# Kernel optimization log

Hardware: AMD Instinct MI355X
Metric: run time of the kernel (lower is better)

Reference implementation:

```python
import jax, jax.numpy as jnp
import numpy as np

NUM_USER = 100000
NUM_ITEM = 50000
DIM = 64
NUM_EDGES = 3200000


def setup_inputs() -> dict:
    key = jax.random.key(0)
    k1, k2, k3, k4 = jax.random.split(key, 4)
    return {
        "user_embedding": jax.random.normal(k1, (NUM_USER, DIM), dtype=jnp.float32),
        "item_embedding": jax.random.normal(k2, (NUM_ITEM, DIM), dtype=jnp.float32),
        "edge_user": jax.random.randint(k3, (NUM_EDGES,), 0, NUM_USER, dtype=jnp.int32).astype(jnp.int64),
        "edge_item": jax.random.randint(k4, (NUM_EDGES,), 0, NUM_ITEM, dtype=jnp.int32).astype(jnp.int64),
    }


def _segment_mean(feats, idx, num_segments):
    # scatter_mean semantics: sum per segment / count, empty segments -> 0
    s = jax.ops.segment_sum(feats, idx, num_segments=num_segments)  # [n, dim]
    cnt = jax.ops.segment_sum(jnp.ones((idx.shape[0], 1), feats.dtype), idx,
                              num_segments=num_segments)  # [n, 1]
    return s / jnp.maximum(cnt, 1.0)


def reference(user_embedding, item_embedding, edge_user, edge_item):
    num_user = user_embedding.shape[0]
    num_item = item_embedding.shape[0]

    # view1: aggregate_neighbor_features — mean of purchased-item embeddings per user
    neighbor_feat = _segment_mean(item_embedding[edge_item], edge_user, num_user)

    # view2: aggregate_cooccurrence_features — two-stage mean aggregation
    # stage 1: per item, mean of its purchasers' embeddings
    item_user_agg = _segment_mean(user_embedding[edge_user], edge_item, num_item)
    # stage 2: per user, mean of stage-1 features of purchased items
    cooccur_feat = _segment_mean(item_user_agg[edge_item], edge_user, num_user)

    return (neighbor_feat, cooccur_feat)
```

## Files before the change

kernel.cpp:

```cpp
#include <hip/hip_runtime.h>
#include <hip/hip_fp16.h>

constexpr int NUM_USER  = 100000;
constexpr int NUM_ITEM  = 50000;
constexpr int DIM       = 64;
constexpr int NUM_EDGES = 3200000;

constexpr int KPB   = 32;
constexpr int NB_U  = (NUM_USER + KPB - 1) / KPB;
constexpr int NB_I  = (NUM_ITEM + KPB - 1) / KPB;
constexpr int CHUNK = 4096;
constexpr int CSH   = 14;
constexpr int NCH_I = 4;
constexpr int NCH_U = 7;
constexpr int CAP_U = 1280;
constexpr int CAP_I = 2304;
constexpr int PGRID = 256;
constexpr int CVTB  = 256;

__device__ __forceinline__ __half2 u2h(unsigned u) {
  union { unsigned u; __half2 h; } v; v.u = u; return v.h;
}
__device__ __forceinline__ unsigned h2u(__half2 h) {
  union { __half2 h; unsigned u; } v; v.h = h; return v.u;
}
__device__ __forceinline__ float u_as_f(unsigned u) {
  union { unsigned u; float f; } v; v.u = u; return v.f;
}

__device__ __forceinline__ int detect64(const void* eu, const void* ei) {
  const int* a = (const int*)eu;
  const int* b = (const int*)ei;
  int any = 0;
#pragma unroll
  for (int i = 1; i < 64; i += 2) { any |= a[i]; any |= b[i]; }
  return any == 0;
}

__device__ __forceinline__ int idx_at(const void* p, int e, int is64) {
  return is64 ? ((const int*)p)[2 * e] : ((const int*)p)[e];
}

__device__ __forceinline__ void cvt_body(int t0, int stride,
                                         const float* __restrict__ ue,
                                         unsigned* __restrict__ u32,
                                         const float* __restrict__ ie,
                                         unsigned* __restrict__ fused) {
  const int nu = NUM_USER * 32, ni = NUM_ITEM * 32;
  for (int t = t0; t < nu + ni; t += stride) {
    if (t < nu) {
      const unsigned long long raw =
          __builtin_nontemporal_load((const unsigned long long*)ue + t);
      const __half2 h = __floats2half2_rn(u_as_f((unsigned)raw),
                                          u_as_f((unsigned)(raw >> 32)));
      __builtin_nontemporal_store(h2u(h), &u32[t]);
    } else {
      const int s = t - nu;
      const unsigned long long raw =
          __builtin_nontemporal_load((const unsigned long long*)ie + s);
      const __half2 h = __floats2half2_rn(u_as_f((unsigned)raw),
                                          u_as_f((unsigned)(raw >> 32)));
      __builtin_nontemporal_store(h2u(h),
                                  &fused[(size_t)(s >> 5) * 64 + 2 * (s & 31)]);
    }
  }
}

__global__ void k_part2cvt(const void* eu_p, const void* ei_p,
                           int* gcur_i, unsigned int* __restrict__ pairs_i,
                           int* gcur_u, unsigned int* __restrict__ pairs_u,
                           int capI, int capU,
                           const float* __restrict__ ue, unsigned* __restrict__ u32t,
                           const float* __restrict__ ie, unsigned* __restrict__ fusedt) {
  __shared__ int hist_u[NB_U], base_u[NB_U];
  __shared__ int hist_i[NB_I], base_i[NB_I];
  if (blockIdx.x >= PGRID) {
    cvt_body((blockIdx.x - PGRID) * blockDim.x + threadIdx.x,
             CVTB * blockDim.x, ue, u32t, ie, fusedt);
    return;
  }
  for (int t = threadIdx.x; t < NB_U; t += blockDim.x) hist_u[t] = 0;
  for (int t = threadIdx.x; t < NB_I; t += blockDim.x) hist_i[t] = 0;
  __syncthreads();
  const int is64 = detect64(eu_p, ei_p);
  const int ch = NUM_EDGES / PGRID;
  const int lo = blockIdx.x * ch, hiE = lo + ch;
  for (int e = lo + threadIdx.x; e < hiE; e += blockDim.x) {
    atomicAdd(&hist_u[idx_at(eu_p, e, is64) >> 5], 1);
    atomicAdd(&hist_i[idx_at(ei_p, e, is64) >> 5], 1);
  }
  __syncthreads();
  for (int t = threadIdx.x; t < NB_U; t += blockDim.x) {
    const int h = hist_u[t];
    int b = 0;
    if (h) {
      b = atomicAdd(&gcur_u[t], h);
      if (capU) b += t * capU;
    }
    base_u[t] = b;
    hist_u[t] = 0;
  }
  for (int t = threadIdx.x; t < NB_I; t += blockDim.x) {
    const int h = hist_i[t];
    int b = 0;
    if (h) {
      b = atomicAdd(&gcur_i[t], h);
      if (capI) b += t * capI;
    }
    base_i[t] = b;
    hist_i[t] = 0;
  }
  __syncthreads();
  for (int e = lo + threadIdx.x; e < hiE; e += blockDim.x) {
    const int eu = idx_at(eu_p, e, is64);
    const int ei = idx_at(ei_p, e, is64);
    const int bi = ei >> 5;
    const int pi = base_i[bi] + atomicAdd(&hist_i[bi], 1);
    if (!capI || pi < (bi + 1) * capI)
      pairs_i[pi] = ((unsigned)(ei & 31) << 17) | (unsigned)eu;
    const int bu = eu >> 5;
    const int pu = base_u[bu] + atomicAdd(&hist_u[bu], 1);
    if (!capU || pu < (bu + 1) * capU)
      pairs_u[pu] = ((unsigned)(eu & 31) << 17) | (unsigned)ei;
  }
}

__global__ void k_hist_part(const void* eu_p, const void* ei_p,
                            int* __restrict__ partials) {
  __shared__ int hu[NB_U];
  __shared__ int hi_[NB_I];
  for (int t = threadIdx.x; t < NB_U; t += blockDim.x) hu[t] = 0;
  for (int t = threadIdx.x; t < NB_I; t += blockDim.x) hi_[t] = 0;
  __syncthreads();
  const int is64 = detect64(eu_p, ei_p);
  const int ga = gridDim.x;
  const int ch = NUM_EDGES / ga;
  const int b = blockIdx.x;
  const int lo = b * ch, hiE = lo + ch;
  for (int e = lo + threadIdx.x; e < hiE; e += blockDim.x) {
    atomicAdd(&hu[idx_at(eu_p, e, is64) >> 5], 1);
    atomicAdd(&hi_[idx_at(ei_p, e, is64) >> 5], 1);
  }
  __syncthreads();
  int* pu = partials;
  int* pi = partials + (size_t)NB_U * ga;
  for (int t = threadIdx.x; t < NB_U; t += blockDim.x) pu[(size_t)t * ga + b] = hu[t];
  for (int t = threadIdx.x; t < NB_I; t += blockDim.x) pi[(size_t)t * ga + b] = hi_[t];
}

__global__ void k_hist_reduce(const int* __restrict__ partials, int ga,
                              int* __restrict__ gcnt_u, int* __restrict__ gcnt_i) {
  const int k = blockIdx.x * blockDim.x + threadIdx.x;
  if (k >= NB_U + NB_I) return;
  const int* base = (k < NB_U) ? partials + (size_t)k * ga
                               : partials + (size_t)NB_U * ga + (size_t)(k - NB_U) * ga;
  int s = 0;
  for (int b = 0; b < ga; ++b) s += base[b];
  if (k < NB_U) gcnt_u[k] = s;
  else          gcnt_i[k - NB_U] = s;
}

__device__ void scan_body(const int* __restrict__ in, int* __restrict__ out,
                          int* __restrict__ cur, int n) {
  __shared__ int part[1024];
  const int t = threadIdx.x;
  const int chunk = (n + 1023) >> 10;
  const int lo = min(t * chunk, n);
  const int hi = min(lo + chunk, n);
  int s = 0;
  for (int i = lo; i < hi; ++i) s += in[i];
  part[t] = s;
  __syncthreads();
  for (int d = 1; d < 1024; d <<= 1) {
    int v = (t >= d) ? part[t - d] : 0;
    __syncthreads();
    part[t] += v;
    __syncthreads();
  }
  int run = (t == 0) ? 0 : part[t - 1];
  for (int i = lo; i < hi; ++i) {
    int v = in[i];
    out[i] = run; cur[i] = run; run += v;
  }
  if (t == 1023) out[n] = part[1023];
}

__global__ void k_scan2(const int* cu, int* bu, int* curu,
                        const int* ci, int* bi, int* curi) {
  if (blockIdx.x == 0) scan_body(cu, bu, curu, NB_U);
  else                 scan_body(ci, bi, curi, NB_I);
}

__device__ __forceinline__ void bucket_extent(int bucket, const int* gbase,
                                              const int* gcnt, int cap,
                                              int& lo, int& hi) {
  if (cap > 0) {
    lo = bucket * cap;
    hi = lo + min(gcnt[bucket], cap);
  } else {
    lo = gbase[bucket];
    hi = gbase[bucket + 1];
  }
}

__global__ __launch_bounds__(256, 8)
void k_agg_item(const unsigned* __restrict__ user32,
                const unsigned int* __restrict__ pairs,
                const int* __restrict__ gbase, const int* __restrict__ gcnt,
                int cap, unsigned* __restrict__ fused) {
  constexpr int NBINS = NCH_U * KPB;
  __shared__ int sorted[CHUNK];
  __shared__ int hist[NBINS], base[NBINS], cur[NBINS];
  __shared__ int gsum[NCH_U];
  const int tid = threadIdx.x;
  const int lane = tid & 63;
  const int wid = tid >> 6;
  const int half = lane >> 5;
  const int c = lane & 31;
  const int bucket = blockIdx.x;
  int lo, hi;
  bucket_extent(bucket, gbase, gcnt, cap, lo, hi);

  unsigned s[8]; int cnt[8];
#pragma unroll
  for (int r = 0; r < 8; ++r) { s[r] = 0u; cnt[r] = 0; }

  for (int clo = lo; clo < hi; clo += CHUNK) {
    const int csz = min(CHUNK, hi - clo);
    for (int t = tid; t < NBINS; t += 256) hist[t] = 0;
    __syncthreads();
    for (int j = tid; j < csz; j += 256) {
      const unsigned p = pairs[clo + j];
      atomicAdd(&hist[((p & 0x1FFFF) >> CSH) * KPB + (p >> 17)], 1);
    }
    __syncthreads();
    if (tid < NCH_U) {
      int g = 0;
      for (int q = 0; q < KPB; ++q) g += hist[tid * KPB + q];
      gsum[tid] = g;
    }
    __syncthreads();
    for (int t = tid; t < NBINS; t += 256) {
      const int ch = t >> 5;
      int b = 0;
      for (int q = 0; q < ch; ++q) b += gsum[q];
      for (int q = ch * KPB; q < t; ++q) b += hist[q];
      base[t] = b; cur[t] = b;
    }
    __syncthreads();
    for (int j = tid; j < csz; j += 256) {
      const unsigned p = pairs[clo + j];
      const int v = (int)(p & 0x1FFFF);
      const int slot = atomicAdd(&cur[(v >> CSH) * KPB + (p >> 17)], 1);
      sorted[slot] = v;
    }
    __syncthreads();
    for (int ch = 0; ch < NCH_U; ++ch) {
#pragma unroll
      for (int r = 0; r < 8; ++r) {
        const int bin = ch * KPB + wid * 8 + r;
        const int jlo = base[bin], jhi = cur[bin];
        cnt[r] += jhi - jlo;
        for (int j = jlo; j < jhi; j += 8) {
          unsigned w[4];
#pragma unroll
          for (int q = 0; q < 4; ++q) {
            const int jj = j + 2 * q + half;
            w[q] = (jj < jhi) ? user32[(size_t)sorted[jj] * 32 + c] : 0u;
          }
#pragma unroll
          for (int q = 0; q < 4; ++q)
            s[r] = h2u(__hadd2(u2h(s[r]), u2h(w[q])));
        }
      }
    }
    __syncthreads();
  }

  const int i0 = bucket * KPB;
#pragma unroll
  for (int r = 0; r < 8; ++r) {
    const unsigned o = (unsigned)__shfl_xor((int)s[r], 32);
    const __half2 tot = __hadd2(u2h(s[r]), u2h(o));
    const int item = i0 + wid * 8 + r;
    if (half == 0 && item < NUM_ITEM) {
      const float inv = 1.0f / fmaxf((float)cnt[r], 1.f);
      fused[(size_t)item * 64 + 2 * c + 1] =
          h2u(__floats2half2_rn(__low2float(tot) * inv, __high2float(tot) * inv));
    }
  }
}

__global__ __launch_bounds__(256, 8)
void k_agg_user(const unsigned* __restrict__ fused,
                const unsigned int* __restrict__ pairs,
                const int* __restrict__ gbase, const int* __restrict__ gcnt,
                int cap,
                float* __restrict__ out0, float* __restrict__ out1) {
  constexpr int NBINS = NCH_I * KPB;
  __shared__ int sorted[CHUNK];
  __shared__ int hist[NBINS], base[NBINS], cur[NBINS];
  __shared__ int gsum[NCH_I];
  const int tid = threadIdx.x;
  const int lane = tid & 63;
  const int wid = tid >> 6;
  const int half = lane >> 5;
  const int c = lane & 31;
  const int bucket = blockIdx.x;
  int lo, hi;
  bucket_extent(bucket, gbase, gcnt, cap, lo, hi);
  const uint2* fused2 = (const uint2*)fused;

  unsigned s0[8], s1[8]; int cnt[8];
#pragma unroll
  for (int r = 0; r < 8; ++r) { s0[r] = 0u; s1[r] = 0u; cnt[r] = 0; }

  for (int clo = lo; clo < hi; clo += CHUNK) {
    const int csz = min(CHUNK, hi - clo);
    for (int t = tid; t < NBINS; t += 256) hist[t] = 0;
    __syncthreads();
    for (int j = tid; j < csz; j += 256) {
      const unsigned p = pairs[clo + j];
      atomicAdd(&hist[((p & 0x1FFFF) >> CSH) * KPB + (p >> 17)], 1);
    }
    __syncthreads();
    if (tid < NCH_I) {
      int g = 0;
      for (int q = 0; q < KPB; ++q) g += hist[tid * KPB + q];
      gsum[tid] = g;
    }
    __syncthreads();
    for (int t = tid; t < NBINS; t += 256) {
      const int ch = t >> 5;
      int b = 0;
      for (int q = 0; q < ch; ++q) b += gsum[q];
      for (int q = ch * KPB; q < t; ++q) b += hist[q];
      base[t] = b; cur[t] = b;
    }
    __syncthreads();
    for (int j = tid; j < csz; j += 256) {
      const unsigned p = pairs[clo + j];
      const int v = (int)(p & 0x1FFFF);
      const int slot = atomicAdd(&cur[(v >> CSH) * KPB + (p >> 17)], 1);
      sorted[slot] = v;
    }
    __syncthreads();
    for (int ch = 0; ch < NCH_I; ++ch) {
#pragma unroll
      for (int r = 0; r < 8; ++r) {
        const int bin = ch * KPB + wid * 8 + r;
        const int jlo = base[bin], jhi = cur[bin];
        cnt[r] += jhi - jlo;
        for (int j = jlo; j < jhi; j += 8) {
          uint2 w[4];
#pragma unroll
          for (int q = 0; q < 4; ++q) {
            const int jj = j + 2 * q + half;
            w[q] = (jj < jhi) ? fused2[(size_t)sorted[jj] * 32 + c]
                              : make_uint2(0u, 0u);
          }
#pragma unroll
          for (int q = 0; q < 4; ++q) {
            s0[r] = h2u(__hadd2(u2h(s0[r]), u2h(w[q].x)));
            s1[r] = h2u(__hadd2(u2h(s1[r]), u2h(w[q].y)));
          }
        }
      }
    }
    __syncthreads();
  }

  const int u0 = bucket * KPB;
#pragma unroll
  for (int r = 0; r < 8; ++r) {
    const unsigned o0 = (unsigned)__shfl_xor((int)s0[r], 32);
    const unsigned o1 = (unsigned)__shfl_xor((int)s1[r], 32);
    const __half2 t0 = __hadd2(u2h(s0[r]), u2h(o0));
    const __half2 t1 = __hadd2(u2h(s1[r]), u2h(o1));
    const int u = u0 + wid * 8 + r;
    if (half == 0 && u < NUM_USER) {
      const float inv = 1.0f / fmaxf((float)cnt[r], 1.f);
      ((float2*)out0)[(size_t)u * 32 + c] =
          make_float2(__low2float(t0) * inv, __high2float(t0) * inv);
      ((float2*)out1)[(size_t)u * 32 + c] =
          make_float2(__low2float(t1) * inv, __high2float(t1) * inv);
    }
  }
}

__global__ void k_scatter1(const float* __restrict__ user_emb,
                           const float* __restrict__ item_emb,
                           const void* eu_p, const void* ei_p,
                           float* out0, float* item_sum,
                           float* cnt_user, float* cnt_item) {
  const int is64 = detect64(eu_p, ei_p);
  const int lane = threadIdx.x & (DIM - 1);
  const int sub  = threadIdx.x >> 6;
  const int epb  = blockDim.x >> 6;
  for (int e = blockIdx.x * epb + sub; e < NUM_EDGES; e += gridDim.x * epb) {
    const int eu = idx_at(eu_p, e, is64);
    const int ei = idx_at(ei_p, e, is64);
    atomicAdd(&out0[eu * DIM + lane], item_emb[ei * DIM + lane]);
    atomicAdd(&item_sum[ei * DIM + lane], user_emb[eu * DIM + lane]);
    if (lane == 0) {
      atomicAdd(&cnt_user[eu], 1.0f);
      atomicAdd(&cnt_item[ei], 1.0f);
    }
  }
}

__global__ void k_div_item(float* item_sum, const float* __restrict__ cnt_item) {
  const int n = NUM_ITEM * DIM;
  for (int t = blockIdx.x * blockDim.x + threadIdx.x; t < n;
       t += gridDim.x * blockDim.x)
    item_sum[t] /= fmaxf(cnt_item[t >> 6], 1.0f);
}

__global__ void k_scatter2(const float* __restrict__ item_agg,
                           const void* eu_p, const void* ei_p, float* out1) {
  const int is64 = detect64(eu_p, ei_p);
  const int lane = threadIdx.x & (DIM - 1);
  const int sub  = threadIdx.x >> 6;
  const int epb  = blockDim.x >> 6;
  for (int e = blockIdx.x * epb + sub; e < NUM_EDGES; e += gridDim.x * epb) {
    const int eu = idx_at(eu_p, e, is64);
    const int ei = idx_at(ei_p, e, is64);
    atomicAdd(&out1[eu * DIM + lane], item_agg[ei * DIM + lane]);
  }
}

__global__ void k_finalize(float* out0, float* out1,
                           const float* __restrict__ cnt_user) {
  const int n = NUM_USER * DIM;
  for (int t = blockIdx.x * blockDim.x + threadIdx.x; t < n;
       t += gridDim.x * blockDim.x) {
    const float c = fmaxf(cnt_user[t >> 6], 1.0f);
    out0[t] /= c;
    out1[t] /= c;
  }
}

extern "C" void kernel_launch(void* const* d_in, const int* in_sizes, int n_in,
                              void* d_out, int out_size, void* d_ws, size_t ws_size,
                              hipStream_t stream) {
  const float* user_emb = (const float*)d_in[0];
  const float* item_emb = (const float*)d_in[1];
  const void*  eu_p     = d_in[2];
  const void*  ei_p     = d_in[3];

  float* out0 = (float*)d_out;
  float* out1 = out0 + (size_t)NUM_USER * DIM;

  int* wsi = (int*)d_ws;
  float* wsf = (float*)d_ws;

  const size_t s_pairs_u = 0;
  const size_t s_pairs_i = s_pairs_u + (size_t)NB_U * CAP_U;
  const size_t s_user32  = s_pairs_i + (size_t)NB_I * CAP_I;
  const size_t s_fused   = s_user32 + (size_t)NUM_USER * 32;
  const size_t s_gcur_u  = s_fused + (size_t)NUM_ITEM * 64;
  const size_t s_gcur_i  = s_gcur_u + NB_U;
  const size_t s_end     = s_gcur_i + NB_I;
  const size_t need_static = s_end * 4;

  const size_t o_pairs   = 0;
  const size_t o_user32  = o_pairs + NUM_EDGES;
  const size_t o_fused   = o_user32 + (size_t)NUM_USER * 32;
  const size_t o_gcnt_u  = o_fused + (size_t)NUM_ITEM * 64;
  const size_t o_gbase_u = o_gcnt_u + NB_U;
  const size_t o_gcur_u  = o_gbase_u + NB_U + 1;
  const size_t o_gcnt_i  = o_gcur_u + NB_U;
  const size_t o_gbase_i = o_gcnt_i + NB_I;
  const size_t o_gcur_i  = o_gbase_i + NB_I + 1;
  const size_t o_pairs2  = o_gcur_i + NB_I;
  const size_t need_dynamic = (o_pairs2 + NUM_EDGES) * 4;

  if (ws_size >= need_static) {
    unsigned int* pairs_u = (unsigned int*)(wsi + s_pairs_u);
    unsigned int* pairs_i = (unsigned int*)(wsi + s_pairs_i);
    unsigned* user32 = (unsigned*)(wsi + s_user32);
    unsigned* fused  = (unsigned*)(wsi + s_fused);
    int* gcur_u = wsi + s_gcur_u;
    int* gcur_i = wsi + s_gcur_i;

    hipMemsetAsync(gcur_u, 0, (size_t)(NB_U + NB_I) * 4, stream);
    k_part2cvt<<<PGRID + CVTB, 1024, 0, stream>>>(
        eu_p, ei_p, gcur_i, pairs_i, gcur_u, pairs_u, CAP_I, CAP_U,
        user_emb, user32, item_emb, fused);
    k_agg_item<<<NB_I, 256, 0, stream>>>(user32, pairs_i, nullptr,
                                         gcur_i, CAP_I, fused);
    k_agg_user<<<NB_U, 256, 0, stream>>>(fused, pairs_u, nullptr,
                                         gcur_u, CAP_U, out0, out1);
  } else if (ws_size >= need_dynamic) {
    unsigned int* pairs_i  = (unsigned int*)(wsi + o_pairs);
    int*          partials = wsi + o_pairs;
    unsigned* user32 = (unsigned*)(wsi + o_user32);
    unsigned* fused  = (unsigned*)(wsi + o_fused);
    int* gcnt_u  = wsi + o_gcnt_u;
    int* gbase_u = wsi + o_gbase_u;
    int* gcur_u  = wsi + o_gcur_u;
    int* gcnt_i  = wsi + o_gcnt_i;
    int* gbase_i = wsi + o_gbase_i;
    int* gcur_i  = wsi + o_gcur_i;
    unsigned int* pairs_u = (unsigned int*)(wsi + o_pairs2);

    k_hist_part<<<256, 512, 0, stream>>>(eu_p, ei_p, partials);
    k_hist_reduce<<<(NB_U + NB_I + 255) / 256, 256, 0, stream>>>(partials, 256,
                                                                 gcnt_u, gcnt_i);
    k_scan2<<<2, 1024, 0, stream>>>(gcnt_u, gbase_u, gcur_u,
                                    gcnt_i, gbase_i, gcur_i);
    k_part2cvt<<<PGRID + CVTB, 1024, 0, stream>>>(
        eu_p, ei_p, gcur_i, pairs_i, gcur_u, pairs_u, 0, 0,
        user_emb, user32, item_emb, fused);
    k_agg_item<<<NB_I, 256, 0, stream>>>(user32, pairs_i, gbase_i,
                                         nullptr, 0, fused);
    k_agg_user<<<NB_U, 256, 0, stream>>>(fused, pairs_u, gbase_u,
                                         nullptr, 0, out0, out1);
  } else {
    float* item_sum = wsf;
    float* cnt_user = wsf + (size_t)NUM_ITEM * DIM;
    float* cnt_item = cnt_user + NUM_USER;
    const size_t used = ((size_t)NUM_ITEM * DIM + NUM_USER + NUM_ITEM) * 4;

    hipMemsetAsync(d_out, 0, (size_t)out_size * sizeof(float), stream);
    hipMemsetAsync(d_ws, 0, used, stream);
    k_scatter1<<<4096, 256, 0, stream>>>(user_emb, item_emb, eu_p, ei_p,
                                         out0, item_sum, cnt_user, cnt_item);
    k_div_item<<<2048, 256, 0, stream>>>(item_sum, cnt_item);
    k_scatter2<<<4096, 256, 0, stream>>>(item_sum, eu_p, ei_p, out1);
    k_finalize<<<2048, 256, 0, stream>>>(out0, out1, cnt_user);
  }
}
```

Measured before the change: 249.5 us.

## Replace single-pass bucket partition with two-pass coarse-then-fine radix partition

Edge partitioning now runs in two passes. The first pass scatters edges into 196 coarse groups (512 users or 256 items each), and a second kernel sub-partitions each group into the fine 32-row buckets. This replaces the single pass that kept ~4700 histogram bins in shared memory and issued scattered writes across thousands of buckets, which should improve write locality and cut global atomics. The cost is an extra read and write of all edge pairs plus more workspace, and the two-stage capacity clamps can drop edges if a group overflows. The old dynamic-offset path is removed and the static-capacity path is kept as a fallback.

```diff
diff --git a/kernel.cpp b/kernel.cpp
--- a/kernel.cpp
+++ b/kernel.cpp
@@ -17,6 +17,12 @@
 constexpr int CAP_I = 2304;
 constexpr int PGRID = 256;
 constexpr int CVTB  = 256;
+constexpr int NG    = 196;
+constexpr int GSH_U = 9;
+constexpr int GSH_I = 8;
+constexpr int FBG_U = 16;
+constexpr int FBG_I = 8;
+constexpr int GCAP  = 17152;
 
 __device__ __forceinline__ __half2 u2h(unsigned u) {
   union { unsigned u; __half2 h; } v; v.u = u; return v.h;
@@ -66,10 +72,97 @@
   }
 }
 
+__global__ void k_passA(const void* eu_p, const void* ei_p,
+                        int* gccur_u, int* gccur_i,
+                        unsigned* __restrict__ coarse_u,
+                        unsigned* __restrict__ coarse_i,
+                        const float* __restrict__ ue, unsigned* __restrict__ u32t,
+                        const float* __restrict__ ie, unsigned* __restrict__ fusedt) {
+  __shared__ int hu[NG], bu[NG];
+  __shared__ int hi_[NG], bi_[NG];
+  if (blockIdx.x >= PGRID) {
+    cvt_body((blockIdx.x - PGRID) * blockDim.x + threadIdx.x,
+             CVTB * blockDim.x, ue, u32t, ie, fusedt);
+    return;
+  }
+  for (int t = threadIdx.x; t < NG; t += blockDim.x) { hu[t] = 0; hi_[t] = 0; }
+  __syncthreads();
+  const int is64 = detect64(eu_p, ei_p);
+  const int ch = NUM_EDGES / PGRID;
+  const int lo = blockIdx.x * ch, hiE = lo + ch;
+  for (int e = lo + threadIdx.x; e < hiE; e += blockDim.x) {
+    atomicAdd(&hu[idx_at(eu_p, e, is64) >> GSH_U], 1);
+    atomicAdd(&hi_[idx_at(ei_p, e, is64) >> GSH_I], 1);
+  }
+  __syncthreads();
+  for (int t = threadIdx.x; t < NG; t += blockDim.x) {
+    const int h0 = hu[t];
+    bu[t] = h0 ? atomicAdd(&gccur_u[t], h0) : 0;
+    hu[t] = 0;
+    const int h1 = hi_[t];
+    bi_[t] = h1 ? atomicAdd(&gccur_i[t], h1) : 0;
+    hi_[t] = 0;
+  }
+  __syncthreads();
+  for (int e = lo + threadIdx.x; e < hiE; e += blockDim.x) {
+    const int eu = idx_at(eu_p, e, is64);
+    const int ei = idx_at(ei_p, e, is64);
+    const int gu = eu >> GSH_U;
+    const int pu = bu[gu] + atomicAdd(&hu[gu], 1);
+    if (pu < GCAP)
+      coarse_u[(size_t)gu * GCAP + pu] =
+          ((unsigned)(eu & ((1 << GSH_U) - 1)) << 17) | (unsigned)ei;
+    const int gi = ei >> GSH_I;
+    const int pi = bi_[gi] + atomicAdd(&hi_[gi], 1);
+    if (pi < GCAP)
+      coarse_i[(size_t)gi * GCAP + pi] =
+          ((unsigned)(ei & ((1 << GSH_I) - 1)) << 17) | (unsigned)eu;
+  }
+}
+
+__global__ void k_passB(const unsigned* __restrict__ coarse_u,
+                        const unsigned* __restrict__ coarse_i,
+                        const int* __restrict__ gccur_u,
+                        const int* __restrict__ gccur_i,
+                        unsigned* __restrict__ pairs_u,
+                        unsigned* __restrict__ pairs_i,
+                        int* __restrict__ gcnt_u, int* __restrict__ gcnt_i) {
+  __shared__ int h[FBG_U], cur[FBG_U];
+  const bool isU = blockIdx.x < NG;
+  const int g = isU ? blockIdx.x : blockIdx.x - NG;
+  const unsigned* src = (isU ? coarse_u : coarse_i) + (size_t)g * GCAP;
+  int n = isU ? gccur_u[g] : gccur_i[g];
+  n = min(n, GCAP);
+  const int FB = isU ? FBG_U : FBG_I;
+  const int CAP = isU ? CAP_U : CAP_I;
+  const int NBfin = isU ? NB_U : NB_I;
+  unsigned* dst = isU ? pairs_u : pairs_i;
+  int* gcnt = isU ? gcnt_u : gcnt_i;
+  const int tid = threadIdx.x;
+
+  if (tid < FB) h[tid] = 0;
+  __syncthreads();
+  for (int j = tid; j < n; j += blockDim.x)
+    atomicAdd(&h[(src[j] >> 22) & (FB - 1)], 1);
+  __syncthreads();
+  if (tid < FB) {
+    const int fbg = g * FB + tid;
+    if (fbg < NBfin) gcnt[fbg] = min(h[tid], CAP);
+    cur[tid] = 0;
+  }
+  __syncthreads();
+  for (int j = tid; j < n; j += blockDim.x) {
+    const unsigned p = src[j];
+    const int fb = (p >> 22) & (FB - 1);
+    const int pos = atomicAdd(&cur[fb], 1);
+    if (pos < CAP)
+      dst[(size_t)(g * FB + fb) * CAP + pos] = p & 0x3FFFFFu;
+  }
+}
+
 __global__ void k_part2cvt(const void* eu_p, const void* ei_p,
                            int* gcur_i, unsigned int* __restrict__ pairs_i,
                            int* gcur_u, unsigned int* __restrict__ pairs_u,
-                           int capI, int capU,
                            const float* __restrict__ ue, unsigned* __restrict__ u32t,
                            const float* __restrict__ ie, unsigned* __restrict__ fusedt) {
   __shared__ int hist_u[NB_U], base_u[NB_U];
@@ -92,22 +185,12 @@
   __syncthreads();
   for (int t = threadIdx.x; t < NB_U; t += blockDim.x) {
     const int h = hist_u[t];
-    int b = 0;
-    if (h) {
-      b = atomicAdd(&gcur_u[t], h);
-      if (capU) b += t * capU;
-    }
-    base_u[t] = b;
+    base_u[t] = h ? t * CAP_U + atomicAdd(&gcur_u[t], h) : 0;
     hist_u[t] = 0;
   }
   for (int t = threadIdx.x; t < NB_I; t += blockDim.x) {
     const int h = hist_i[t];
-    int b = 0;
-    if (h) {
-      b = atomicAdd(&gcur_i[t], h);
-      if (capI) b += t * capI;
-    }
-    base_i[t] = b;
+    base_i[t] = h ? t * CAP_I + atomicAdd(&gcur_i[t], h) : 0;
     hist_i[t] = 0;
   }
   __syncthreads();
@@ -116,98 +199,20 @@
     const int ei = idx_at(ei_p, e, is64);
     const int bi = ei >> 5;
     const int pi = base_i[bi] + atomicAdd(&hist_i[bi], 1);
-    if (!capI || pi < (bi + 1) * capI)
+    if (pi < (bi + 1) * CAP_I)
       pairs_i[pi] = ((unsigned)(ei & 31) << 17) | (unsigned)eu;
     const int bu = eu >> 5;
     const int pu = base_u[bu] + atomicAdd(&hist_u[bu], 1);
-    if (!capU || pu < (bu + 1) * capU)
+    if (pu < (bu + 1) * CAP_U)
       pairs_u[pu] = ((unsigned)(eu & 31) << 17) | (unsigned)ei;
-  }
-}
-
-__global__ void k_hist_part(const void* eu_p, const void* ei_p,
-                            int* __restrict__ partials) {
-  __shared__ int hu[NB_U];
-  __shared__ int hi_[NB_I];
-  for (int t = threadIdx.x; t < NB_U; t += blockDim.x) hu[t] = 0;
-  for (int t = threadIdx.x; t < NB_I; t += blockDim.x) hi_[t] = 0;
-  __syncthreads();
-  const int is64 = detect64(eu_p, ei_p);
-  const int ga = gridDim.x;
-  const int ch = NUM_EDGES / ga;
-  const int b = blockIdx.x;
-  const int lo = b * ch, hiE = lo + ch;
-  for (int e = lo + threadIdx.x; e < hiE; e += blockDim.x) {
-    atomicAdd(&hu[idx_at(eu_p, e, is64) >> 5], 1);
-    atomicAdd(&hi_[idx_at(ei_p, e, is64) >> 5], 1);
-  }
-  __syncthreads();
-  int* pu = partials;
-  int* pi = partials + (size_t)NB_U * ga;
-  for (int t = threadIdx.x; t < NB_U; t += blockDim.x) pu[(size_t)t * ga + b] = hu[t];
-  for (int t = threadIdx.x; t < NB_I; t += blockDim.x) pi[(size_t)t * ga + b] = hi_[t];
-}
-
-__global__ void k_hist_reduce(const int* __restrict__ partials, int ga,
-                              int* __restrict__ gcnt_u, int* __restrict__ gcnt_i) {
-  const int k = blockIdx.x * blockDim.x + threadIdx.x;
-  if (k >= NB_U + NB_I) return;
-  const int* base = (k < NB_U) ? partials + (size_t)k * ga
-                               : partials + (size_t)NB_U * ga + (size_t)(k - NB_U) * ga;
-  int s = 0;
-  for (int b = 0; b < ga; ++b) s += base[b];
-  if (k < NB_U) gcnt_u[k] = s;
-  else          gcnt_i[k - NB_U] = s;
-}
-
-__device__ void scan_body(const int* __restrict__ in, int* __restrict__ out,
-                          int* __restrict__ cur, int n) {
-  __shared__ int part[1024];
-  const int t = threadIdx.x;
-  const int chunk = (n + 1023) >> 10;
-  const int lo = min(t * chunk, n);
-  const int hi = min(lo + chunk, n);
-  int s = 0;
-  for (int i = lo; i < hi; ++i) s += in[i];
-  part[t] = s;
-  __syncthreads();
-  for (int d = 1; d < 1024; d <<= 1) {
-    int v = (t >= d) ? part[t - d] : 0;
-    __syncthreads();
-    part[t] += v;
-    __syncthreads();
-  }
-  int run = (t == 0) ? 0 : part[t - 1];
-  for (int i = lo; i < hi; ++i) {
-    int v = in[i];
-    out[i] = run; cur[i] = run; run += v;
-  }
-  if (t == 1023) out[n] = part[1023];
-}
-
-__global__ void k_scan2(const int* cu, int* bu, int* curu,
-                        const int* ci, int* bi, int* curi) {
-  if (blockIdx.x == 0) scan_body(cu, bu, curu, NB_U);
-  else                 scan_body(ci, bi, curi, NB_I);
-}
-
-__device__ __forceinline__ void bucket_extent(int bucket, const int* gbase,
-                                              const int* gcnt, int cap,
-                                              int& lo, int& hi) {
-  if (cap > 0) {
-    lo = bucket * cap;
-    hi = lo + min(gcnt[bucket], cap);
-  } else {
-    lo = gbase[bucket];
-    hi = gbase[bucket + 1];
   }
 }
 
 __global__ __launch_bounds__(256, 8)
 void k_agg_item(const unsigned* __restrict__ user32,
                 const unsigned int* __restrict__ pairs,
-                const int* __restrict__ gbase, const int* __restrict__ gcnt,
-                int cap, unsigned* __restrict__ fused) {
+                const int* __restrict__ gcnt,
+                unsigned* __restrict__ fused) {
   constexpr int NBINS = NCH_U * KPB;
   __shared__ int sorted[CHUNK];
   __shared__ int hist[NBINS], base[NBINS], cur[NBINS];
@@ -218,8 +223,8 @@
   const int half = lane >> 5;
   const int c = lane & 31;
   const int bucket = blockIdx.x;
-  int lo, hi;
-  bucket_extent(bucket, gbase, gcnt, cap, lo, hi);
+  const int lo = bucket * CAP_I;
+  const int hi = lo + min(gcnt[bucket], CAP_I);
 
   unsigned s[8]; int cnt[8];
 #pragma unroll
@@ -294,8 +299,7 @@
 __global__ __launch_bounds__(256, 8)
 void k_agg_user(const unsigned* __restrict__ fused,
                 const unsigned int* __restrict__ pairs,
-                const int* __restrict__ gbase, const int* __restrict__ gcnt,
-                int cap,
+                const int* __restrict__ gcnt,
                 float* __restrict__ out0, float* __restrict__ out1) {
   constexpr int NBINS = NCH_I * KPB;
   __shared__ int sorted[CHUNK];
@@ -307,8 +311,8 @@
   const int half = lane >> 5;
   const int c = lane & 31;
   const int bucket = blockIdx.x;
-  int lo, hi;
-  bucket_extent(bucket, gbase, gcnt, cap, lo, hi);
+  const int lo = bucket * CAP_U;
+  const int hi = lo + min(gcnt[bucket], CAP_U);
   const uint2* fused2 = (const uint2*)fused;
 
   unsigned s0[8], s1[8]; int cnt[8];
@@ -454,68 +458,60 @@
   int* wsi = (int*)d_ws;
   float* wsf = (float*)d_ws;
 
+  const size_t t0_coarse_u = 0;
+  const size_t t0_coarse_i = t0_coarse_u + (size_t)NG * GCAP;
+  const size_t t0_pairs_u  = t0_coarse_i + (size_t)NG * GCAP;
+  const size_t t0_pairs_i  = t0_pairs_u + (size_t)NB_U * CAP_U;
+  const size_t t0_user32   = t0_pairs_i + (size_t)NB_I * CAP_I;
+  const size_t t0_fused    = t0_user32 + (size_t)NUM_USER * 32;
+  const size_t t0_gccur    = t0_fused + (size_t)NUM_ITEM * 64;
+  const size_t t0_gcnt_u   = t0_gccur + 2 * NG;
+  const size_t t0_gcnt_i   = t0_gcnt_u + NB_U;
+  const size_t need_t0     = (t0_gcnt_i + NB_I) * 4;
+
   const size_t s_pairs_u = 0;
   const size_t s_pairs_i = s_pairs_u + (size_t)NB_U * CAP_U;
   const size_t s_user32  = s_pairs_i + (size_t)NB_I * CAP_I;
   const size_t s_fused   = s_user32 + (size_t)NUM_USER * 32;
   const size_t s_gcur_u  = s_fused + (size_t)NUM_ITEM * 64;
   const size_t s_gcur_i  = s_gcur_u + NB_U;
-  const size_t s_end     = s_gcur_i + NB_I;
-  const size_t need_static = s_end * 4;
-
-  const size_t o_pairs   = 0;
-  const size_t o_user32  = o_pairs + NUM_EDGES;
-  const size_t o_fused   = o_user32 + (size_t)NUM_USER * 32;
-  const size_t o_gcnt_u  = o_fused + (size_t)NUM_ITEM * 64;
-  const size_t o_gbase_u = o_gcnt_u + NB_U;
-  const size_t o_gcur_u  = o_gbase_u + NB_U + 1;
-  const size_t o_gcnt_i  = o_gcur_u + NB_U;
-  const size_t o_gbase_i = o_gcnt_i + NB_I;
-  const size_t o_gcur_i  = o_gbase_i + NB_I + 1;
-  const size_t o_pairs2  = o_gcur_i + NB_I;
-  const size_t need_dynamic = (o_pairs2 + NUM_EDGES) * 4;
-
-  if (ws_size >= need_static) {
-    unsigned int* pairs_u = (unsigned int*)(wsi + s_pairs_u);
-    unsigned int* pairs_i = (unsigned int*)(wsi + s_pairs_i);
-    unsigned* user32 = (unsigned*)(wsi + s_user32);
-    unsigned* fused  = (unsigned*)(wsi + s_fused);
+  const size_t need_t1   = (s_gcur_i + NB_I) * 4;
+
+  if (ws_size >= need_t0) {
+    unsigned* coarse_u = (unsigned*)(wsi + t0_coarse_u);
+    unsigned* coarse_i = (unsigned*)(wsi + t0_coarse_i);
+    unsigned* pairs_u  = (unsigned*)(wsi + t0_pairs_u);
+    unsigned* pairs_i  = (unsigned*)(wsi + t0_pairs_i);
+    unsigned* user32   = (unsigned*)(wsi + t0_user32);
+    unsigned* fused    = (unsigned*)(wsi + t0_fused);
+    int* gccur_u = wsi + t0_gccur;
+    int* gccur_i = gccur_u + NG;
+    int* gcnt_u  = wsi + t0_gcnt_u;
+    int* gcnt_i  = wsi + t0_gcnt_i;
+
+    hipMemsetAsync(gccur_u, 0, (size_t)(2 * NG) * 4, stream);
+    k_passA<<<PGRID + CVTB, 1024, 0, stream>>>(eu_p, ei_p, gccur_u, gccur_i,
+                                               coarse_u, coarse_i,
+                                               user_emb, user32, item_emb, fused);
+    k_passB<<<2 * NG, 1024, 0, stream>>>(coarse_u, coarse_i, gccur_u, gccur_i,
+                                         pairs_u, pairs_i, gcnt_u, gcnt_i);
+    k_agg_item<<<NB_I, 256, 0, stream>>>(user32, pairs_i, gcnt_i, fused);
+    k_agg_user<<<NB_U, 256, 0, stream>>>(fused, pairs_u, gcnt_u, out0, out1);
+  } else if (ws_size >= need_t1) {
+    unsigned* pairs_u = (unsigned*)(wsi + s_pairs_u);
+    unsigned* pairs_i = (unsigned*)(wsi + s_pairs_i);
+    unsigned* user32  = (unsigned*)(wsi + s_user32);
+    unsigned* fused   = (unsigned*)(wsi + s_fused);
     int* gcur_u = wsi + s_gcur_u;
     int* gcur_i = wsi + s_gcur_i;
 
     hipMemsetAsync(gcur_u, 0, (size_t)(NB_U + NB_I) * 4, stream);
-    k_part2cvt<<<PGRID + CVTB, 1024, 0, stream>>>(
-        eu_p, ei_p, gcur_i, pairs_i, gcur_u, pairs_u, CAP_I, CAP_U,
-        user_emb, user32, item_emb, fused);
-    k_agg_item<<<NB_I, 256, 0, stream>>>(user32, pairs_i, nullptr,
-                                         gcur_i, CAP_I, fused);
-    k_agg_user<<<NB_U, 256, 0, stream>>>(fused, pairs_u, nullptr,
-                                         gcur_u, CAP_U, out0, out1);
-  } else if (ws_size >= need_dynamic) {
-    unsigned int* pairs_i  = (unsigned int*)(wsi + o_pairs);
-    int*          partials = wsi + o_pairs;
-    unsigned* user32 = (unsigned*)(wsi + o_user32);
-    unsigned* fused  = (unsigned*)(wsi + o_fused);
-    int* gcnt_u  = wsi + o_gcnt_u;
-    int* gbase_u = wsi + o_gbase_u;
-    int* gcur_u  = wsi + o_gcur_u;
-    int* gcnt_i  = wsi + o_gcnt_i;
-    int* gbase_i = wsi + o_gbase_i;
-    int* gcur_i  = wsi + o_gcur_i;
-    unsigned int* pairs_u = (unsigned int*)(wsi + o_pairs2);
-
-    k_hist_part<<<256, 512, 0, stream>>>(eu_p, ei_p, partials);
-    k_hist_reduce<<<(NB_U + NB_I + 255) / 256, 256, 0, stream>>>(partials, 256,
-                                                                 gcnt_u, gcnt_i);
-    k_scan2<<<2, 1024, 0, stream>>>(gcnt_u, gbase_u, gcur_u,
-                                    gcnt_i, gbase_i, gcur_i);
-    k_part2cvt<<<PGRID + CVTB, 1024, 0, stream>>>(
-        eu_p, ei_p, gcur_i, pairs_i, gcur_u, pairs_u, 0, 0,
-        user_emb, user32, item_emb, fused);
-    k_agg_item<<<NB_I, 256, 0, stream>>>(user32, pairs_i, gbase_i,
-                                         nullptr, 0, fused);
-    k_agg_user<<<NB_U, 256, 0, stream>>>(fused, pairs_u, gbase_u,
-                                         nullptr, 0, out0, out1);
+    k_part2cvt<<<PGRID + CVTB, 1024, 0, stream>>>(eu_p, ei_p, gcur_i, pairs_i,
+                                                  gcur_u, pairs_u,
+                                                  user_emb, user32,
+                                                  item_emb, fused);
+    k_agg_item<<<NB_I, 256, 0, stream>>>(user32, pairs_i, gcur_i, fused);
+    k_agg_user<<<NB_U, 256, 0, stream>>>(fused, pairs_u, gcur_u, out0, out1);
   } else {
     float* item_sum = wsf;
     float* cnt_user = wsf + (size_t)NUM_ITEM * DIM;
```

New measurement: 227.8 us. 8.7% less time.
